# Performance work log

Hardware: AMD Instinct MI355X
Metric: run time of the kernel (lower is better)

## Reference

```python
import jax, jax.numpy as jnp
import numpy as np

T, H, I = 32768, 2048, 768  # tokens, hidden_size, moe_intermediate_size


def setup_inputs() -> dict:
    key = jax.random.key(0)
    k1, k2, k3 = jax.random.split(key, 3)
    hidden_states = jax.random.normal(k1, (T, H), dtype=jnp.float32)
    # merged gate_up weight: columns [0:I] = gate, [I:2I] = up
    w_gate_up = jax.random.normal(k2, (H, 2 * I), dtype=jnp.float32) * 0.02
    w_down = jax.random.normal(k3, (I, H), dtype=jnp.float32) * 0.02
    return {"hidden_states": hidden_states, "w_gate_up": w_gate_up, "w_down": w_down}


def reference(hidden_states, w_gate_up, w_down):
    # gate_up projection: [T, H] @ [H, 2I] -> [T, 2I]
    gate_up = jnp.einsum('th,hf->tf', hidden_states, w_gate_up)
    gate, up = jnp.split(gate_up, 2, axis=-1)
    # SiluAndMul: silu(gate) * up -> [T, I]
    x = jax.nn.silu(gate) * up
    # down projection: [T, I] @ [I, H] -> [T, H]
    return jnp.einsum('ti,ih->th', x, w_down)
```

## Files before the change

### kernel.cpp

```cpp
#include <hip/hip_runtime.h>

#define T_TOK 32768
#define H_DIM 2048
#define I_DIM 768
#define N1_DIM 1536

typedef unsigned short ushort_t;
typedef __attribute__((ext_vector_type(8))) short  short8;
typedef __attribute__((ext_vector_type(4))) float  floatx4;

__device__ __forceinline__ ushort_t f2bf(float f) {
    union { float f; unsigned u; } v; v.f = f;
    unsigned u = v.u;
    unsigned r = (u + 0x7fffu + ((u >> 16) & 1u)) >> 16;
    return (ushort_t)r;
}

typedef __attribute__((address_space(1))) const void gq_t;
typedef __attribute__((address_space(3))) void lq_t;
__device__ __forceinline__ void gld_lds16(const void* g, void* l) {
    __builtin_amdgcn_global_load_lds((gq_t*)g, (lq_t*)l, 16, 0, 0);
}

__global__ __launch_bounds__(256) void cast_f32_bf16_k(
    const float* __restrict__ in, ushort_t* __restrict__ out)
{
    size_t i = ((size_t)blockIdx.x * 256 + threadIdx.x) * 8;
    const float4 a = *(const float4*)(in + i);
    const float4 b = *(const float4*)(in + i + 4);
    short8 o;
    o[0] = (short)f2bf(a.x); o[1] = (short)f2bf(a.y);
    o[2] = (short)f2bf(a.z); o[3] = (short)f2bf(a.w);
    o[4] = (short)f2bf(b.x); o[5] = (short)f2bf(b.y);
    o[6] = (short)f2bf(b.z); o[7] = (short)f2bf(b.w);
    *(short8*)(out + i) = o;
}

__device__ __forceinline__ int gu_perm(int c) {
    const int t  = (c >= I_DIM) ? 1 : 0;
    const int cc = c - t * I_DIM;
    return ((cc >> 4) << 5) + (t << 4) + (cc & 15);
}

template <bool PERM>
__global__ __launch_bounds__(256) void transpose_cast_k(
    const float* __restrict__ in, ushort_t* __restrict__ out, int R, int C)
{
    __shared__ float tile[32][33];
    const int c0 = blockIdx.x * 32;
    const int r0 = blockIdx.y * 32;
    const int tx = threadIdx.x;
    const int ty = threadIdx.y;
#pragma unroll
    for (int dy = 0; dy < 32; dy += 8)
        tile[ty + dy][tx] = in[(size_t)(r0 + ty + dy) * C + (c0 + tx)];
    __syncthreads();
#pragma unroll
    for (int dy = 0; dy < 32; dy += 8) {
        const int c = c0 + ty + dy;
        const int orow = PERM ? gu_perm(c) : c;
        out[(size_t)orow * R + (r0 + tx)] = f2bf(tile[tx][ty + dy]);
    }
}

#define GB    __builtin_amdgcn_s_barrier()
#define SB0   __builtin_amdgcn_sched_barrier(0)
#define LGKM0 asm volatile("s_waitcnt lgkmcnt(0)" ::: "memory")
#define VMW(N) asm volatile("s_waitcnt vmcnt(" #N ")" ::: "memory")

template <int EPI, int NBN>
__global__ __launch_bounds__(512, 2) void gemm_bt8(
    const ushort_t* __restrict__ A,
    const ushort_t* __restrict__ Bt,
    void* __restrict__ Cv,
    int lda, int ldb, int ldc, int K)
{
    __shared__ __align__(16) ushort_t lds[65536];

    const int tid  = threadIdx.x;
    const int lane = tid & 63;
    const int wave = tid >> 6;
    const int wm   = (wave >> 2) * 128;
    const int wn   = (wave & 3) * 64;
    const int s    = lane & 15;
    const int q    = lane >> 4;
    const int s7   = s & 7;

    const int nwg = gridDim.x;
    const int cpx = nwg >> 3;
    const int wg  = blockIdx.x;
    const int swz = (wg & 7) * cpx + (wg >> 3);
    const int mb  = swz / NBN;
    const int m0  = mb * 256;
    const int n0  = (swz - mb * NBN) * 256;

    const int r3 = lane >> 3;
    const int sk = ((lane & 7) ^ r3) * 8;
    const ushort_t* Ab = A  + (size_t)(m0 + wave * 8 + r3) * lda + sk;
    const ushort_t* Bb = Bt + (size_t)(n0 + wave * 8 + r3) * ldb + sk;

#define STAGE_A(kt, ofs, b) gld_lds16(Ab + (size_t)((ofs) * 8) * lda + (kt), \
                                      &lds[(b) * 16384 + (wave + (ofs)) * 512])
#define STAGE_B(kt, ofs, b) gld_lds16(Bb + (size_t)((ofs) * 8) * ldb + (kt), \
                                      &lds[32768 + (b) * 16384 + (wave + (ofs)) * 512])

    const int arow = wm + s;
    const int brow = wn + s;
#define LDA4(b, ks, mh, av) { _Pragma("unroll") for (int ii = 0; ii < 4; ++ii) \
    av[ii] = *(const short8*)&lds[(b) * 16384 + (arow + (mh) * 64 + ii * 16) * 64 \
                                  + (((ks) * 4 + q) ^ s7) * 8]; }
#define LDB4(b, ks, bv) { _Pragma("unroll") for (int jj = 0; jj < 4; ++jj) \
    bv[jj] = *(const short8*)&lds[32768 + (b) * 16384 + (brow + jj * 16) * 64 \
                                  + (((ks) * 4 + q) ^ s7) * 8]; }
#define MFMA16(mh, av, bv) { _Pragma("unroll") for (int ii = 0; ii < 4; ++ii) \
    _Pragma("unroll") for (int jj = 0; jj < 4; ++jj) \
        acc[(mh) * 4 + ii][jj] = __builtin_amdgcn_mfma_f32_16x16x32_bf16( \
            av[ii], bv[jj], acc[(mh) * 4 + ii][jj], 0, 0, 0); }

    floatx4 acc[8][4];
#pragma unroll
    for (int i = 0; i < 8; ++i)
#pragma unroll
        for (int j = 0; j < 4; ++j)
            acc[i][j] = floatx4{0.f, 0.f, 0.f, 0.f};

    const int NT = K >> 6;

    STAGE_A(0, 0, 0);  STAGE_A(0, 16, 0);
    STAGE_B(0, 0, 0);  STAGE_B(0, 8, 0);
    STAGE_B(0, 16, 0); STAGE_B(0, 24, 0);
    STAGE_A(0, 8, 0);  STAGE_A(0, 24, 0);
    VMW(2);
    GB; SB0;

    for (int t = 0; t < NT - 1; ++t) {
        const int b   = t & 1;
        const int nb  = b ^ 1;
        const int kt1 = (t + 1) << 6;
        short8 av[4], bv[4];
        LDA4(b, 0, 0, av); LDB4(b, 0, bv);
        STAGE_A(kt1, 0, nb); STAGE_A(kt1, 16, nb);
        GB; LGKM0; SB0;
        __builtin_amdgcn_s_setprio(1); MFMA16(0, av, bv); __builtin_amdgcn_s_setprio(0);
        VMW(2);
        GB;
        LDA4(b, 0, 1, av);
        STAGE_B(kt1, 0, nb); STAGE_B(kt1, 8, nb);
        GB; LGKM0; SB0;
        __builtin_amdgcn_s_setprio(1); MFMA16(1, av, bv); __builtin_amdgcn_s_setprio(0);
        GB;
        LDA4(b, 1, 0, av); LDB4(b, 1, bv);
        STAGE_B(kt1, 16, nb); STAGE_B(kt1, 24, nb);
        GB; LGKM0; SB0;
        __builtin_amdgcn_s_setprio(1); MFMA16(0, av, bv); __builtin_amdgcn_s_setprio(0);
        GB;
        LDA4(b, 1, 1, av);
        STAGE_A(kt1, 8, nb); STAGE_A(kt1, 24, nb);
        GB; LGKM0; SB0;
        __builtin_amdgcn_s_setprio(1); MFMA16(1, av, bv); __builtin_amdgcn_s_setprio(0);
        VMW(2);
        GB;
    }
    {
        const int b = (NT - 1) & 1;
        short8 av[4], bv[4];
        LDA4(b, 0, 0, av); LDB4(b, 0, bv);
        GB; LGKM0; SB0;
        __builtin_amdgcn_s_setprio(1); MFMA16(0, av, bv); __builtin_amdgcn_s_setprio(0);
        VMW(0);
        GB;
        LDA4(b, 0, 1, av);
        GB; LGKM0; SB0;
        __builtin_amdgcn_s_setprio(1); MFMA16(1, av, bv); __builtin_amdgcn_s_setprio(0);
        GB;
        LDA4(b, 1, 0, av); LDB4(b, 1, bv);
        GB; LGKM0; SB0;
        __builtin_amdgcn_s_setprio(1); MFMA16(0, av, bv); __builtin_amdgcn_s_setprio(0);
        GB;
        LDA4(b, 1, 1, av);
        LGKM0; SB0;
        __builtin_amdgcn_s_setprio(1); MFMA16(1, av, bv); __builtin_amdgcn_s_setprio(0);
    }

    if (EPI == 0) {
        float* C = (float*)Cv;
#pragma unroll
        for (int i = 0; i < 8; ++i) {
            const int r = m0 + wm + i * 16 + q * 4;
#pragma unroll
            for (int j = 0; j < 4; ++j) {
                const int cn = n0 + wn + j * 16 + s;
#pragma unroll
                for (int tt = 0; tt < 4; ++tt)
                    C[(size_t)(r + tt) * ldc + cn] = acc[i][j][tt];
            }
        }
    } else {
        ushort_t* X = (ushort_t*)Cv;
        const int cb2 = (n0 + wn) >> 1;
#pragma unroll
        for (int i = 0; i < 8; ++i) {
            const int r = m0 + wm + i * 16 + q * 4;
#pragma unroll
            for (int jp = 0; jp < 2; ++jp) {
                const int cn = cb2 + jp * 16 + s;
#pragma unroll
                for (int tt = 0; tt < 4; ++tt) {
                    const float g  = acc[i][2 * jp][tt];
                    const float u  = acc[i][2 * jp + 1][tt];
                    const float sv = g / (1.0f + __expf(-g));
                    X[(size_t)(r + tt) * ldc + cn] = f2bf(sv * u);
                }
            }
        }
    }
#undef STAGE_A
#undef STAGE_B
#undef LDA4
#undef LDB4
#undef MFMA16
}

extern "C" void kernel_launch(void* const* d_in, const int* in_sizes, int n_in,
                              void* d_out, int out_size, void* d_ws, size_t ws_size,
                              hipStream_t stream)
{
    const float* hs  = (const float*)d_in[0];
    const float* wgu = (const float*)d_in[1];
    const float* wd  = (const float*)d_in[2];
    float*       out = (float*)d_out;

    char* ws = (char*)d_ws;
    ushort_t* wgu_t = (ushort_t*)ws;
    ushort_t* wd_t  = (ushort_t*)(ws + 6291456);
    ushort_t* xb    = (ushort_t*)(ws + 9437184);

    ushort_t* hs_b = (ushort_t*)d_out;

    cast_f32_bf16_k<<<32768, 256, 0, stream>>>(hs, hs_b);
    transpose_cast_k<true><<<dim3(N1_DIM / 32, H_DIM / 32), dim3(32, 8), 0, stream>>>(
        wgu, wgu_t, H_DIM, N1_DIM);
    transpose_cast_k<false><<<dim3(H_DIM / 32, I_DIM / 32), dim3(32, 8), 0, stream>>>(
        wd, wd_t, I_DIM, H_DIM);
    gemm_bt8<1, 6><<<(T_TOK / 256) * (N1_DIM / 256), 512, 0, stream>>>(
        hs_b, wgu_t, (void*)xb, H_DIM, H_DIM, I_DIM, H_DIM);
    gemm_bt8<0, 8><<<(T_TOK / 256) * (H_DIM / 256), 512, 0, stream>>>(
        xb, wd_t, (void*)out, I_DIM, I_DIM, H_DIM, I_DIM);
}
```

Before: 716.3 us.

## Fuse hidden-state bf16 cast into gate_up GEMM A-tile staging

```diff
diff --git a/kernel.cpp b/kernel.cpp
--- a/kernel.cpp
+++ b/kernel.cpp
@@ -22,18 +22,10 @@
     __builtin_amdgcn_global_load_lds((gq_t*)g, (lq_t*)l, 16, 0, 0);
 }
 
-__global__ __launch_bounds__(256) void cast_f32_bf16_k(
-    const float* __restrict__ in, ushort_t* __restrict__ out)
-{
-    size_t i = ((size_t)blockIdx.x * 256 + threadIdx.x) * 8;
-    const float4 a = *(const float4*)(in + i);
-    const float4 b = *(const float4*)(in + i + 4);
-    short8 o;
-    o[0] = (short)f2bf(a.x); o[1] = (short)f2bf(a.y);
-    o[2] = (short)f2bf(a.z); o[3] = (short)f2bf(a.w);
-    o[4] = (short)f2bf(b.x); o[5] = (short)f2bf(b.y);
-    o[6] = (short)f2bf(b.z); o[7] = (short)f2bf(b.w);
-    *(short8*)(out + i) = o;
+__device__ __forceinline__ void cvtpk4(float x0, float x1, float x2, float x3,
+                                       unsigned& w0, unsigned& w1) {
+    asm("v_cvt_pk_bf16_f32 %0, %1, %2" : "=v"(w0) : "v"(x0), "v"(x1));
+    asm("v_cvt_pk_bf16_f32 %0, %1, %2" : "=v"(w1) : "v"(x2), "v"(x3));
 }
 
 __device__ __forceinline__ int gu_perm(int c) {
@@ -68,11 +60,11 @@
 #define LGKM0 asm volatile("s_waitcnt lgkmcnt(0)" ::: "memory")
 #define VMW(N) asm volatile("s_waitcnt vmcnt(" #N ")" ::: "memory")
 
-template <int EPI, int NBN>
+template <int NBN>
 __global__ __launch_bounds__(512, 2) void gemm_bt8(
     const ushort_t* __restrict__ A,
     const ushort_t* __restrict__ Bt,
-    void* __restrict__ Cv,
+    float* __restrict__ C,
     int lda, int ldb, int ldc, int K)
 {
     __shared__ __align__(16) ushort_t lds[65536];
@@ -182,39 +174,168 @@
         __builtin_amdgcn_s_setprio(1); MFMA16(1, av, bv); __builtin_amdgcn_s_setprio(0);
     }
 
-    if (EPI == 0) {
-        float* C = (float*)Cv;
-#pragma unroll
-        for (int i = 0; i < 8; ++i) {
-            const int r = m0 + wm + i * 16 + q * 4;
-#pragma unroll
-            for (int j = 0; j < 4; ++j) {
-                const int cn = n0 + wn + j * 16 + s;
-#pragma unroll
-                for (int tt = 0; tt < 4; ++tt)
-                    C[(size_t)(r + tt) * ldc + cn] = acc[i][j][tt];
+#pragma unroll
+    for (int i = 0; i < 8; ++i) {
+        const int r = m0 + wm + i * 16 + q * 4;
+#pragma unroll
+        for (int j = 0; j < 4; ++j) {
+            const int cn = n0 + wn + j * 16 + s;
+#pragma unroll
+            for (int tt = 0; tt < 4; ++tt)
+                C[(size_t)(r + tt) * ldc + cn] = acc[i][j][tt];
+        }
+    }
+#undef STAGE_A
+#undef STAGE_B
+#undef LDA4
+#undef LDB4
+#undef MFMA16
+}
+
+template <int NBN>
+__global__ __launch_bounds__(512, 2) void gemm1_fused(
+    const float* __restrict__ A,
+    const ushort_t* __restrict__ Bt,
+    ushort_t* __restrict__ X)
+{
+    __shared__ __align__(16) ushort_t lds[65536];
+
+    const int tid  = threadIdx.x;
+    const int lane = tid & 63;
+    const int wave = tid >> 6;
+    const int wm   = (wave >> 2) * 128;
+    const int wn   = (wave & 3) * 64;
+    const int s    = lane & 15;
+    const int q    = lane >> 4;
+    const int s7   = s & 7;
+
+    const int nwg = gridDim.x;
+    const int cpx = nwg >> 3;
+    const int wg  = blockIdx.x;
+    const int swz = (wg & 7) * cpx + (wg >> 3);
+    const int mb  = swz / NBN;
+    const int m0  = mb * 256;
+    const int n0  = (swz - mb * NBN) * 256;
+
+    const int r3 = lane >> 3;
+    const int sk = ((lane & 7) ^ r3) * 8;
+    const float*    Af = A  + (size_t)(m0 + wave * 8 + r3) * H_DIM + sk;
+    const ushort_t* Bb = Bt + (size_t)(n0 + wave * 8 + r3) * H_DIM + sk;
+
+#define LOADF(kt, ofs, fa, fb) { \
+    fa = *(const float4*)(Af + (size_t)((ofs) * 8) * H_DIM + (kt)); \
+    fb = *(const float4*)(Af + (size_t)((ofs) * 8) * H_DIM + (kt) + 4); }
+#define WRITEF(ofs, b, fa, fb) { unsigned w0_, w1_, w2_, w3_; \
+    cvtpk4(fa.x, fa.y, fa.z, fa.w, w0_, w1_); \
+    cvtpk4(fb.x, fb.y, fb.z, fb.w, w2_, w3_); \
+    *(uint4*)&lds[(b) * 16384 + (wave + (ofs)) * 512 + lane * 8] = \
+        make_uint4(w0_, w1_, w2_, w3_); }
+#define STAGE_B(kt, ofs, b) gld_lds16(Bb + (size_t)((ofs) * 8) * H_DIM + (kt), \
+                                      &lds[32768 + (b) * 16384 + (wave + (ofs)) * 512])
+
+    const int arow = wm + s;
+    const int brow = wn + s;
+#define LDA4(b, ks, mh, av) { _Pragma("unroll") for (int ii = 0; ii < 4; ++ii) \
+    av[ii] = *(const short8*)&lds[(b) * 16384 + (arow + (mh) * 64 + ii * 16) * 64 \
+                                  + (((ks) * 4 + q) ^ s7) * 8]; }
+#define LDB4(b, ks, bv) { _Pragma("unroll") for (int jj = 0; jj < 4; ++jj) \
+    bv[jj] = *(const short8*)&lds[32768 + (b) * 16384 + (brow + jj * 16) * 64 \
+                                  + (((ks) * 4 + q) ^ s7) * 8]; }
+#define MFMA16(mh, av, bv) { _Pragma("unroll") for (int ii = 0; ii < 4; ++ii) \
+    _Pragma("unroll") for (int jj = 0; jj < 4; ++jj) \
+        acc[(mh) * 4 + ii][jj] = __builtin_amdgcn_mfma_f32_16x16x32_bf16( \
+            av[ii], bv[jj], acc[(mh) * 4 + ii][jj], 0, 0, 0); }
+
+    floatx4 acc[8][4];
+#pragma unroll
+    for (int i = 0; i < 8; ++i)
+#pragma unroll
+        for (int j = 0; j < 4; ++j)
+            acc[i][j] = floatx4{0.f, 0.f, 0.f, 0.f};
+
+    const int NT = H_DIM >> 6;
+    float4 a0, a1, a2, a3;
+    float4 c0, c1, c2, c3;
+
+    LOADF(0, 0, a0, a1);  LOADF(0, 16, a2, a3);
+    LOADF(0, 8, c0, c1);  LOADF(0, 24, c2, c3);
+    STAGE_B(0, 0, 0);  STAGE_B(0, 8, 0);
+    STAGE_B(0, 16, 0); STAGE_B(0, 24, 0);
+    VMW(8);  WRITEF(0, 0, a0, a1);  WRITEF(16, 0, a2, a3);
+    VMW(4);  WRITEF(8, 0, c0, c1);  WRITEF(24, 0, c2, c3);
+    VMW(0);
+    LGKM0; GB; SB0;
+
+    for (int t = 0; t < NT - 1; ++t) {
+        const int b   = t & 1;
+        const int nb  = b ^ 1;
+        const int kt1 = (t + 1) << 6;
+        short8 av[4], bv[4];
+        LDA4(b, 0, 0, av); LDB4(b, 0, bv);
+        LOADF(kt1, 0, a0, a1); LOADF(kt1, 16, a2, a3);
+        GB; LGKM0; SB0;
+        __builtin_amdgcn_s_setprio(1); MFMA16(0, av, bv); __builtin_amdgcn_s_setprio(0);
+        GB;
+        LDA4(b, 0, 1, av);
+        LOADF(kt1, 8, c0, c1); LOADF(kt1, 24, c2, c3);
+        STAGE_B(kt1, 0, nb); STAGE_B(kt1, 8, nb);
+        GB; LGKM0; SB0;
+        __builtin_amdgcn_s_setprio(1); MFMA16(1, av, bv); __builtin_amdgcn_s_setprio(0);
+        GB;
+        LDA4(b, 1, 0, av); LDB4(b, 1, bv);
+        STAGE_B(kt1, 16, nb); STAGE_B(kt1, 24, nb);
+        GB; LGKM0; SB0;
+        __builtin_amdgcn_s_setprio(1); MFMA16(0, av, bv); __builtin_amdgcn_s_setprio(0);
+        VMW(8);
+        WRITEF(0, nb, a0, a1); WRITEF(16, nb, a2, a3);
+        GB;
+        LDA4(b, 1, 1, av);
+        GB; LGKM0; SB0;
+        __builtin_amdgcn_s_setprio(1); MFMA16(1, av, bv); __builtin_amdgcn_s_setprio(0);
+        VMW(4);
+        WRITEF(8, nb, c0, c1); WRITEF(24, nb, c2, c3);
+        VMW(0);
+        LGKM0;
+        GB;
+    }
+    {
+        const int b = (NT - 1) & 1;
+        short8 av[4], bv[4];
+        LDA4(b, 0, 0, av); LDB4(b, 0, bv);
+        GB; LGKM0; SB0;
+        __builtin_amdgcn_s_setprio(1); MFMA16(0, av, bv); __builtin_amdgcn_s_setprio(0);
+        GB;
+        LDA4(b, 0, 1, av);
+        GB; LGKM0; SB0;
+        __builtin_amdgcn_s_setprio(1); MFMA16(1, av, bv); __builtin_amdgcn_s_setprio(0);
+        GB;
+        LDA4(b, 1, 0, av); LDB4(b, 1, bv);
+        GB; LGKM0; SB0;
+        __builtin_amdgcn_s_setprio(1); MFMA16(0, av, bv); __builtin_amdgcn_s_setprio(0);
+        GB;
+        LDA4(b, 1, 1, av);
+        LGKM0; SB0;
+        __builtin_amdgcn_s_setprio(1); MFMA16(1, av, bv); __builtin_amdgcn_s_setprio(0);
+    }
+
+    const int cb2 = (n0 + wn) >> 1;
+#pragma unroll
+    for (int i = 0; i < 8; ++i) {
+        const int r = m0 + wm + i * 16 + q * 4;
+#pragma unroll
+        for (int jp = 0; jp < 2; ++jp) {
+            const int cn = cb2 + jp * 16 + s;
+#pragma unroll
+            for (int tt = 0; tt < 4; ++tt) {
+                const float g  = acc[i][2 * jp][tt];
+                const float u  = acc[i][2 * jp + 1][tt];
+                const float sv = g / (1.0f + __expf(-g));
+                X[(size_t)(r + tt) * I_DIM + cn] = f2bf(sv * u);
             }
         }
-    } else {
-        ushort_t* X = (ushort_t*)Cv;
-        const int cb2 = (n0 + wn) >> 1;
-#pragma unroll
-        for (int i = 0; i < 8; ++i) {
-            const int r = m0 + wm + i * 16 + q * 4;
-#pragma unroll
-            for (int jp = 0; jp < 2; ++jp) {
-                const int cn = cb2 + jp * 16 + s;
-#pragma unroll
-                for (int tt = 0; tt < 4; ++tt) {
-                    const float g  = acc[i][2 * jp][tt];
-                    const float u  = acc[i][2 * jp + 1][tt];
-                    const float sv = g / (1.0f + __expf(-g));
-                    X[(size_t)(r + tt) * ldc + cn] = f2bf(sv * u);
-                }
-            }
-        }
-    }
-#undef STAGE_A
+    }
+#undef LOADF
+#undef WRITEF
 #undef STAGE_B
 #undef LDA4
 #undef LDB4
@@ -235,15 +356,12 @@
     ushort_t* wd_t  = (ushort_t*)(ws + 6291456);
     ushort_t* xb    = (ushort_t*)(ws + 9437184);
 
-    ushort_t* hs_b = (ushort_t*)d_out;
-
-    cast_f32_bf16_k<<<32768, 256, 0, stream>>>(hs, hs_b);
     transpose_cast_k<true><<<dim3(N1_DIM / 32, H_DIM / 32), dim3(32, 8), 0, stream>>>(
         wgu, wgu_t, H_DIM, N1_DIM);
     transpose_cast_k<false><<<dim3(H_DIM / 32, I_DIM / 32), dim3(32, 8), 0, stream>>>(
         wd, wd_t, I_DIM, H_DIM);
-    gemm_bt8<1, 6><<<(T_TOK / 256) * (N1_DIM / 256), 512, 0, stream>>>(
-        hs_b, wgu_t, (void*)xb, H_DIM, H_DIM, I_DIM, H_DIM);
-    gemm_bt8<0, 8><<<(T_TOK / 256) * (H_DIM / 256), 512, 0, stream>>>(
-        xb, wd_t, (void*)out, I_DIM, I_DIM, H_DIM, I_DIM);
-}
+    gemm1_fused<6><<<(T_TOK / 256) * (N1_DIM / 256), 512, 0, stream>>>(
+        hs, wgu_t, xb);
+    gemm_bt8<8><<<(T_TOK / 256) * (H_DIM / 256), 512, 0, stream>>>(
+        xb, wd_t, out, I_DIM, I_DIM, H_DIM, I_DIM);
+}
```

Result: slower. 736.6 us (+2.8%).
